# Performance work log

Hardware: AMD Instinct MI355X
Metric: run time of the kernel (lower is better)

The kernel has to match this reference:

```python
import jax, jax.numpy as jnp
import numpy as np

OMEGA_0 = 32.5
L_SEQ = 512
L_EVAL = 512
C_IN = 16
C_OUT = 16
HIDDEN = 32


def _wn(v, g):
    # torch weight_norm with dim=0: W = g * v / ||v||_row
    return g[:, None] * v / jnp.linalg.norm(v, axis=1, keepdims=True)


def setup_inputs() -> dict:
    key = jax.random.key(0)
    ks = jax.random.split(key, 9)
    x = jax.random.normal(ks[0], (L_SEQ, C_IN), dtype=jnp.float32)
    t = jnp.arange(L_SEQ, dtype=jnp.float32) / L_SEQ
    t_eval = jnp.arange(L_EVAL, dtype=jnp.float32) / L_EVAL
    # SIREN layer 1 (1 -> H), weight-normalized
    v1 = jax.random.normal(ks[1], (HIDDEN, 1), dtype=jnp.float32)
    g1 = jax.random.uniform(ks[2], (HIDDEN,), dtype=jnp.float32, minval=0.5, maxval=1.5)
    b1 = jax.random.normal(ks[3], (HIDDEN,), dtype=jnp.float32) * 0.1
    # SIREN layer 2 (H -> H), weight-normalized
    v2 = jax.random.normal(ks[4], (HIDDEN, HIDDEN), dtype=jnp.float32)
    g2 = jax.random.uniform(ks[5], (HIDDEN,), dtype=jnp.float32, minval=0.5, maxval=1.5)
    b2 = jax.random.normal(ks[6], (HIDDEN,), dtype=jnp.float32) * 0.1
    # final linear (H -> C_in*C_out)
    lim = 1.0 / np.sqrt(HIDDEN)
    W3 = jax.random.uniform(ks[7], (C_OUT * C_IN, HIDDEN), dtype=jnp.float32, minval=-lim, maxval=lim)
    b3 = jax.random.uniform(ks[8], (C_OUT * C_IN,), dtype=jnp.float32, minval=-lim, maxval=lim)
    return {"x": x, "t": t, "t_eval": t_eval,
            "v1": v1, "g1": g1, "b1": b1,
            "v2": v2, "g2": g2, "b2": b2,
            "W3": W3, "b3": b3}


def reference(x, t, t_eval, v1, g1, b1, v2, g2, b2, W3, b3):
    Le, L = t_eval.shape[0], t.shape[0]
    # relative positions: rel[e, s] = t[s] - t_eval[e]
    rel = t[None, :] - t_eval[:, None]                 # (Le, L)
    h = rel.reshape(-1, 1)                             # (Le*L, 1)
    h = jnp.sin(OMEGA_0 * (h @ _wn(v1, g1).T + b1))    # (Le*L, H)
    h = jnp.sin(OMEGA_0 * (h @ _wn(v2, g2).T + b2))    # (Le*L, H)
    k = h @ W3.T + b3                                  # (Le*L, C_out*C_in)
    # output column j = g*C_in + c corresponds to (out channel g, in channel c)
    k = k.reshape(Le, L, C_OUT, C_IN)
    # causal mask: only positions with t[s] <= t_eval[e] contribute
    k = k * (rel <= 0.0).astype(k.dtype)[:, :, None, None]
    # Toeplitz-matvec equivalent: out[e, g] = sum_{s, c} k[e, s, g, c] * x[s, c]
    return jnp.einsum('esgc,sc->eg', k, x)             # (Le, C_out)
```

## Files before the change

kernel.cpp:

```cpp
#include <hip/hip_runtime.h>
#include <math.h>


#define OMEGA0 32.5f

__global__ __launch_bounds__(256) void ck_prep(
    const float* __restrict__ x,
    const float* __restrict__ v1,
    const float* __restrict__ g1,
    const float* __restrict__ b1,
    const float* __restrict__ v2,
    const float* __restrict__ g2,
    const float* __restrict__ b2,
    const float* __restrict__ W3,
    const float* __restrict__ b3,
    float* __restrict__ ws,
    float* __restrict__ out)
{
    const int bid = blockIdx.x;
    const int tid = threadIdx.x;
    float* A  = ws;
    float* Ht = ws + 512*512;
    float* B  = ws + 512*512 + 544*32;

    if (bid < 128) {
        const int sl   = tid >> 6;
        const int lane = tid & 63;
        const int g    = lane >> 2;
        const int oct  = lane & 3;
        const int s    = bid*4 + sl;

        const float4 x0 = *(const float4*)(x + s*16 + 0);
        const float4 x1 = *(const float4*)(x + s*16 + 4);
        const float4 x2 = *(const float4*)(x + s*16 + 8);
        const float4 x3 = *(const float4*)(x + s*16 + 12);
        const float xr[16] = {x0.x,x0.y,x0.z,x0.w, x1.x,x1.y,x1.z,x1.w,
                              x2.x,x2.y,x2.z,x2.w, x3.x,x3.y,x3.z,x3.w};

        float4 o0 = make_float4(0.f,0.f,0.f,0.f);
        float4 o1 = make_float4(0.f,0.f,0.f,0.f);
        #pragma unroll
        for (int c = 0; c < 16; ++c) {
            const float4 w0 = *(const float4*)(W3 + (g*16 + c)*32 + 8*oct);
            const float4 w1 = *(const float4*)(W3 + (g*16 + c)*32 + 8*oct + 4);
            const float xv = xr[c];
            o0.x = fmaf(xv, w0.x, o0.x); o0.y = fmaf(xv, w0.y, o0.y);
            o0.z = fmaf(xv, w0.z, o0.z); o0.w = fmaf(xv, w0.w, o0.w);
            o1.x = fmaf(xv, w1.x, o1.x); o1.y = fmaf(xv, w1.y, o1.y);
            o1.z = fmaf(xv, w1.z, o1.z); o1.w = fmaf(xv, w1.w, o1.w);
        }
        float4* Adst = (float4*)(A + s*512 + g*32 + 8*oct);
        Adst[0] = o0;
        Adst[1] = o1;

        if (tid < 64) {
            const int sb = bid*4 + (tid >> 4);
            const int gb = tid & 15;
            float accB = 0.f;
            #pragma unroll
            for (int c = 0; c < 16; ++c)
                accB = fmaf(b3[gb*16 + c], x[sb*16 + c], accB);
            B[sb*16 + gb] = accB;
            out[bid*64 + tid] = 0.f;
        }
    } else {
        __shared__ float h1s[16][32];
        const int r0 = (bid - 128) * 16;

        #pragma unroll
        for (int u = 0; u < 2; ++u) {
            const int id  = tid + u*256;
            const int row = id >> 5;
            const int k   = id & 31;
            const float w1k = copysignf(g1[k], v1[k]);
            const float rel = (float)(r0 + row - 511) * (1.0f/512.0f);
            h1s[row][k] = __sinf(OMEGA0 * fmaf(rel, w1k, b1[k]));
        }
        __syncthreads();

        const int j  = tid & 31;
        const int rp = tid >> 5;
        float4 v2q[8];
        #pragma unroll
        for (int c = 0; c < 8; ++c)
            v2q[c] = *(const float4*)(v2 + j*32 + 4*c);
        float nrm = 0.f;
        #pragma unroll
        for (int c = 0; c < 8; ++c)
            nrm += v2q[c].x*v2q[c].x + v2q[c].y*v2q[c].y
                 + v2q[c].z*v2q[c].z + v2q[c].w*v2q[c].w;
        const float scale = g2[j] / sqrtf(nrm);
        const float b2j = b2[j];

        #pragma unroll
        for (int rr = 0; rr < 2; ++rr) {
            const int row  = rp*2 + rr;
            const int grow = r0 + row;
            float pre = 0.f;
            #pragma unroll
            for (int c = 0; c < 8; ++c) {
                const float4 h = *(const float4*)&h1s[row][4*c];
                pre += v2q[c].x*h.x + v2q[c].y*h.y + v2q[c].z*h.z + v2q[c].w*h.w;
            }
            const float val = __sinf(OMEGA0 * fmaf(scale, pre, b2j));
            Ht[grow*32 + j] = (grow <= 511) ? val : 0.f;
        }
    }
}

__global__ __launch_bounds__(128) void ck_main(const float* __restrict__ ws,
                                               float* __restrict__ out)
{
    const int et = blockIdx.y;
    const int sc = blockIdx.x;
    const int e0 = et * 8;
    const int s0 = sc * 16;
    if (s0 >= e0 + 8) return;
    const int sEnd = min(s0 + 16, e0 + 8);

    const int tid = threadIdx.x;
    const int g = tid >> 3;
    const int l = tid & 7;

    const float4* A4 = reinterpret_cast<const float4*>(ws);
    const float4* H4 = reinterpret_cast<const float4*>(ws + 512*512);
    const float*  B  = ws + 512*512 + 544*32;

    const int ib = 504 - e0;
    const float4* Ap = A4 + (g*8 + l);

    float4 r[8];
    #pragma unroll
    for (int m = 0; m < 8; ++m) r[m] = H4[(ib + s0 + m)*8 + l];

    float4 aC[8], aN[8];
    #pragma unroll
    for (int j = 0; j < 8; ++j) aC[j] = Ap[(s0 + j)*128];

    float4 acc[8];
    #pragma unroll
    for (int k = 0; k < 8; ++k) acc[k] = make_float4(0.f,0.f,0.f,0.f);

    for (int s = s0; s < sEnd; s += 8) {
        const bool more = (s + 8 < sEnd);
        if (more) {
            #pragma unroll
            for (int j = 0; j < 8; ++j) aN[j] = Ap[(s + 8 + j)*128];
        }
        #pragma unroll
        for (int j = 0; j < 8; ++j) {
            const float4 a = aC[j];
            #pragma unroll
            for (int k = 0; k < 8; ++k) {
                const float4 h = r[(j + 7 - k) & 7];
                acc[k].x = fmaf(a.x, h.x, acc[k].x);
                acc[k].y = fmaf(a.y, h.y, acc[k].y);
                acc[k].z = fmaf(a.z, h.z, acc[k].z);
                acc[k].w = fmaf(a.w, h.w, acc[k].w);
            }
            r[j] = H4[(ib + s + j + 8)*8 + l];
        }
        if (more) {
            #pragma unroll
            for (int j = 0; j < 8; ++j) aC[j] = aN[j];
        }
    }

    float tot[8];
    #pragma unroll
    for (int k = 0; k < 8; ++k) {
        float v = (acc[k].x + acc[k].y) + (acc[k].z + acc[k].w);
        v += __shfl_xor(v, 1);
        v += __shfl_xor(v, 2);
        v += __shfl_xor(v, 4);
        tot[k] = v;
    }
    float mytot = 0.f;
    #pragma unroll
    for (int k = 0; k < 8; ++k) mytot = (l == k) ? tot[k] : mytot;

    const int e = e0 + l;
    float bsum = 0.f;
    #pragma unroll
    for (int q = 0; q < 16; ++q) {
        const int s = s0 + q;
        bsum += (s <= e) ? B[s*16 + g] : 0.f;
    }

    atomicAdd(&out[e*16 + g], mytot + bsum);
}

extern "C" void kernel_launch(void* const* d_in, const int* in_sizes, int n_in,
                              void* d_out, int out_size, void* d_ws, size_t ws_size,
                              hipStream_t stream)
{
    const float* x  = (const float*)d_in[0];
    const float* v1 = (const float*)d_in[3];
    const float* g1 = (const float*)d_in[4];
    const float* b1 = (const float*)d_in[5];
    const float* v2 = (const float*)d_in[6];
    const float* g2 = (const float*)d_in[7];
    const float* b2 = (const float*)d_in[8];
    const float* W3 = (const float*)d_in[9];
    const float* b3 = (const float*)d_in[10];
    float* out = (float*)d_out;
    float* ws  = (float*)d_ws;

    hipLaunchKernelGGL(ck_prep, dim3(162), dim3(256), 0, stream,
                       x, v1, g1, b1, v2, g2, b2, W3, b3, ws, out);

    hipLaunchKernelGGL(ck_main, dim3(32, 64), dim3(128), 0, stream, ws, out);
}
```

Before: 19.15 us.

## Pair triangular tiles per block row and split s-chunk across two half-blocks

The main kernel's grid drops from a 32x64 grid, where roughly half the blocks exit early, to a 33x32 grid that maps two complementary rows of the triangle (p and 63-p) into one grid row, so no launched block is wasted. Each block now has 256 threads, and the two 128-thread halves each handle 8 of the 16 source positions. The halves are combined through shared memory before a single atomicAdd, which replaces the inner loop and its double-buffered A prefetch. This aims to cut launch and scheduling overhead from empty blocks and to add parallelism per tile, at the cost of a __syncthreads and shared-memory exchange.

```diff
diff --git a/kernel.cpp b/kernel.cpp
--- a/kernel.cpp
+++ b/kernel.cpp
@@ -108,62 +108,56 @@
     }
 }
 
-__global__ __launch_bounds__(128) void ck_main(const float* __restrict__ ws,
+__global__ __launch_bounds__(256) void ck_main(const float* __restrict__ ws,
                                                float* __restrict__ out)
 {
-    const int et = blockIdx.y;
-    const int sc = blockIdx.x;
+    const int p  = blockIdx.y;
+    const int xq = blockIdx.x;
+    const int nA = (p >> 1) + 1;
+    const int et = (xq < nA) ? p  : 63 - p;
+    const int sc = (xq < nA) ? xq : xq - nA;
+
     const int e0 = et * 8;
     const int s0 = sc * 16;
-    if (s0 >= e0 + 8) return;
-    const int sEnd = min(s0 + 16, e0 + 8);
 
     const int tid = threadIdx.x;
-    const int g = tid >> 3;
     const int l = tid & 7;
+    const int g = (tid >> 3) & 15;
+    const int h = tid >> 7;
 
     const float4* A4 = reinterpret_cast<const float4*>(ws);
     const float4* H4 = reinterpret_cast<const float4*>(ws + 512*512);
     const float*  B  = ws + 512*512 + 544*32;
 
     const int ib = 504 - e0;
+    const int sb = s0 + 8*h;
     const float4* Ap = A4 + (g*8 + l);
 
     float4 r[8];
     #pragma unroll
-    for (int m = 0; m < 8; ++m) r[m] = H4[(ib + s0 + m)*8 + l];
-
-    float4 aC[8], aN[8];
-    #pragma unroll
-    for (int j = 0; j < 8; ++j) aC[j] = Ap[(s0 + j)*128];
+    for (int m = 0; m < 8; ++m) r[m] = H4[(ib + sb + m)*8 + l];
+
+    float4 a[8];
+    #pragma unroll
+    for (int j = 0; j < 8; ++j) a[j] = Ap[(sb + j)*128];
 
     float4 acc[8];
     #pragma unroll
     for (int k = 0; k < 8; ++k) acc[k] = make_float4(0.f,0.f,0.f,0.f);
 
-    for (int s = s0; s < sEnd; s += 8) {
-        const bool more = (s + 8 < sEnd);
-        if (more) {
-            #pragma unroll
-            for (int j = 0; j < 8; ++j) aN[j] = Ap[(s + 8 + j)*128];
-        }
-        #pragma unroll
-        for (int j = 0; j < 8; ++j) {
-            const float4 a = aC[j];
-            #pragma unroll
-            for (int k = 0; k < 8; ++k) {
-                const float4 h = r[(j + 7 - k) & 7];
-                acc[k].x = fmaf(a.x, h.x, acc[k].x);
-                acc[k].y = fmaf(a.y, h.y, acc[k].y);
-                acc[k].z = fmaf(a.z, h.z, acc[k].z);
-                acc[k].w = fmaf(a.w, h.w, acc[k].w);
-            }
-            r[j] = H4[(ib + s + j + 8)*8 + l];
-        }
-        if (more) {
-            #pragma unroll
-            for (int j = 0; j < 8; ++j) aC[j] = aN[j];
-        }
+    #pragma unroll
+    for (int j = 0; j < 8; ++j) {
+        const float4 av = a[j];
+        #pragma unroll
+        for (int k = 0; k < 8; ++k) {
+            const float4 hv = r[(j + 7 - k) & 7];
+            acc[k].x = fmaf(av.x, hv.x, acc[k].x);
+            acc[k].y = fmaf(av.y, hv.y, acc[k].y);
+            acc[k].z = fmaf(av.z, hv.z, acc[k].z);
+            acc[k].w = fmaf(av.w, hv.w, acc[k].w);
+        }
+        if (j < 7)
+            r[j & 7] = H4[(ib + sb + j + 8)*8 + l];
     }
 
     float tot[8];
@@ -182,12 +176,16 @@
     const int e = e0 + l;
     float bsum = 0.f;
     #pragma unroll
-    for (int q = 0; q < 16; ++q) {
-        const int s = s0 + q;
+    for (int q = 0; q < 8; ++q) {
+        const int s = sb + q;
         bsum += (s <= e) ? B[s*16 + g] : 0.f;
     }
-
-    atomicAdd(&out[e*16 + g], mytot + bsum);
+    const float val = mytot + bsum;
+
+    __shared__ float part[128];
+    if (h == 1) part[tid - 128] = val;
+    __syncthreads();
+    if (h == 0) atomicAdd(&out[e*16 + g], val + part[tid]);
 }
 
 extern "C" void kernel_launch(void* const* d_in, const int* in_sizes, int n_in,
@@ -209,5 +207,5 @@
     hipLaunchKernelGGL(ck_prep, dim3(162), dim3(256), 0, stream,
                        x, v1, g1, b1, v2, g2, b2, W3, b3, ws, out);
 
-    hipLaunchKernelGGL(ck_main, dim3(32, 64), dim3(128), 0, stream, ws, out);
+    hipLaunchKernelGGL(ck_main, dim3(33, 32), dim3(256), 0, stream, ws, out);
 }
```

Result: faster. 18.57 us (-3.0%).
